# Performance work log

Measured on AMD Instinct MI355X. Metric: run time of the kernel, lower is better.

## Reference

```python
import jax, jax.numpy as jnp
import numpy as np

SLOT_SIZE = 64
START_IDX = 0  # slot2idx['<start>']
STOP_IDX = 1   # slot2idx['<stop>']
NEG_INF = -10000.0


def setup_inputs() -> dict:
    key = jax.random.key(0)
    k1, k2 = jax.random.split(key)
    B, T, S = 512, 512, SLOT_SIZE
    logits = jax.random.normal(k1, (B, T, S), dtype=jnp.float32)
    masks = jnp.ones((B, T), dtype=jnp.float32)
    # nn.Parameter(torch.randn(S, S)) with START/STOP constraints from __init__
    transitions = jax.random.normal(k2, (S, S), dtype=jnp.float32)
    transitions = transitions.at[START_IDX, :].set(NEG_INF)
    transitions = transitions.at[:, STOP_IDX].set(NEG_INF)
    return {"logits": logits, "masks": masks, "transitions": transitions}


def reference(logits, masks, transitions):
    """Faithful CRF.forward == _viterbi_decode(logits, masks).

    Replicates the original quirks:
      - masks multiply only the emission feat (transitions are NOT masked
        inside the Viterbi recursion);
      - path_score is taken from the LAST next_tag's (next_tag = S-1)
        score vector at the final timestep, and the backtrace is seeded
        from that same column's argmax;
      - the backtrace re-applies the last backpointer table once before
        walking backwards (exactly as the torch loop does), and the
        popped start tag is dropped, giving a (B, T-1) path.
    """
    B, T, S = logits.shape
    init = jnp.full((B, S), NEG_INF, dtype=logits.dtype).at[:, START_IDX].set(0.0)

    # masked emissions for timesteps 1..T-1, time-major for scan: (T-1, B, S)
    feats = jnp.swapaxes(logits[:, 1:, :] * masks[:, 1:, None], 0, 1)

    def step(fv, feat_t):
        # scores[b, next, prev] = fv[b, prev] + transitions[next, prev]
        scores = fv[:, None, :] + transitions[None, :, :]  # (B, S, S)
        bptr = jnp.argmax(scores, axis=2).astype(jnp.int32)  # (B, S)
        vmax = jnp.max(scores, axis=2)                       # (B, S)
        return vmax + feat_t, (bptr, vmax)

    _, (bptrs, vmaxs) = jax.lax.scan(step, init, feats)  # (T-1, B, S) each

    # torch quirk: next_tag_var / best_tag_id left over from next_tag = S-1
    path_score = vmaxs[-1][:, S - 1]          # (B,)
    t0 = bptrs[-1][:, S - 1]                  # (B,) seed for backtrace

    def back(tag, bp):
        new_tag = jnp.take_along_axis(bp, tag[:, None], axis=1)[:, 0]
        return new_tag, tag  # emit the tag BEFORE following the pointer

    # reverse scan walks bptrs from last to first; emitted ys land at their
    # original time index, so ys == reversed best_path (start tag dropped
    # because the final carry -- the start tag -- is never emitted).
    _, ys = jax.lax.scan(back, t0, bptrs, reverse=True)  # (T-1, B)
    best_seq = jnp.swapaxes(ys, 0, 1)  # (B, T-1)
    return path_score, best_seq
```

## Files before the change

### kernel.cpp

```cpp
#include <hip/hip_runtime.h>


constexpr int Bz = 512;
constexpr int Tz = 512;
constexpr int Sz = 64;
constexpr float NEGINF = -10000.0f;

__device__ __forceinline__ float rlf(float x, int lane) {
    return __int_as_float(__builtin_amdgcn_readlane(__float_as_int(x), lane));
}

__global__ __launch_bounds__(256)
void crf_viterbi_kernel(const float* __restrict__ logits,
                        const float* __restrict__ masks,
                        const float* __restrict__ trans,
                        float* __restrict__ out)
{
    const int n = threadIdx.x & 63;
    const int w = threadIdx.x >> 6;
    const int b = blockIdx.x;
    const int pbase = w * 16;

    __shared__ unsigned bp[128 * 64];
    __shared__ float pval[2][4][64];
    __shared__ int   pidx[2][4][64];
    __shared__ float ys[Tz - 1];

    float tr[16];
    const float4* tr4 = reinterpret_cast<const float4*>(trans + n * 64 + pbase);
    #pragma unroll
    for (int k = 0; k < 4; ++k) {
        float4 v = tr4[k];
        tr[4 * k + 0] = v.x;
        tr[4 * k + 1] = v.y;
        tr[4 * k + 2] = v.z;
        tr[4 * k + 3] = v.w;
    }

    float fv = (n == 0) ? 0.0f : NEGINF;

    const float* lgbase = logits + (size_t)b * Tz * Sz;
    const float* mkbase = masks + (size_t)b * Tz;

    float lg_next = lgbase[1 * Sz + n];
    unsigned pk = 0;
    float psc = 0.0f;

    #pragma unroll 4
    for (int i = 0; i < Tz - 1; ++i) {
        float lg = lg_next;
        int t2 = (i + 2 < Tz) ? (i + 2) : (Tz - 1);
        lg_next = lgbase[t2 * Sz + n];
        float mk = mkbase[i + 1];

        float v[16];
        #pragma unroll
        for (int j = 0; j < 16; ++j)
            v[j] = rlf(fv, pbase + j) + tr[j];

        float mv[2];
        int   mi[2];
        #pragma unroll
        for (int c = 0; c < 2; ++c) {
            int p0 = 8 * c;
            mv[c] = v[p0];
            mi[c] = pbase + p0;
            #pragma unroll
            for (int j = 1; j < 8; ++j) {
                float x = v[p0 + j];
                bool gt = x > mv[c];
                mi[c] = gt ? (pbase + p0 + j) : mi[c];
                mv[c] = gt ? x : mv[c];
            }
        }
        {
            bool gt = mv[1] > mv[0];
            mi[0] = gt ? mi[1] : mi[0];
            mv[0] = gt ? mv[1] : mv[0];
        }

        const int buf = i & 1;
        pval[buf][w][n] = mv[0];
        pidx[buf][w][n] = mi[0];
        __syncthreads();

        float c0 = pval[buf][0][n], c1 = pval[buf][1][n];
        float c2 = pval[buf][2][n], c3 = pval[buf][3][n];
        int   j0 = pidx[buf][0][n], j1 = pidx[buf][1][n];
        int   j2 = pidx[buf][2][n], j3 = pidx[buf][3][n];

        bool g1 = c1 > c0;  float m01 = g1 ? c1 : c0;  int k01 = g1 ? j1 : j0;
        bool g3 = c3 > c2;  float m23 = g3 ? c3 : c2;  int k23 = g3 ? j3 : j2;
        bool gm = m23 > m01;
        float maxv = gm ? m23 : m01;
        int   maxi = gm ? k23 : k01;

        if (i == Tz - 2) psc = maxv;

        if (w == 0) {
            pk |= ((unsigned)maxi) << (8 * (i & 3));
            if ((i & 3) == 3) {
                bp[(i >> 2) * 64 + n] = pk;
                pk = 0;
            }
        }
        fv = maxv + lg * mk;
    }
    if (w == 0) bp[127 * 64 + n] = pk;
    if (w == 0 && n == 63) out[b] = psc;

    __syncthreads();

    if (w == 0) {
        unsigned wcur = bp[127 * 64 + n];
        int w127_63 = __builtin_amdgcn_readlane((int)wcur, 63);
        int tag = (w127_63 >> 16) & 255;

        for (int g = 127; g >= 0; --g) {
            unsigned wnext = (g > 0) ? bp[(g - 1) * 64 + n] : 0u;
            int smax = (g == 127) ? 2 : 3;
            for (int s = smax; s >= 0; --s) {
                int idx = 4 * g + s;
                if (n == 0) ys[idx] = (float)tag;
                int wd = __builtin_amdgcn_readlane((int)wcur, tag);
                tag = (wd >> (8 * s)) & 255;
            }
            wcur = wnext;
        }
    }

    __syncthreads();

    float* outseq = out + Bz + (size_t)b * (Tz - 1);
    for (int k = threadIdx.x; k < Tz - 1; k += 256) outseq[k] = ys[k];
}

extern "C" void kernel_launch(void* const* d_in, const int* in_sizes, int n_in,
                              void* d_out, int out_size, void* d_ws, size_t ws_size,
                              hipStream_t stream) {
    const float* logits = (const float*)d_in[0];
    const float* masks  = (const float*)d_in[1];
    const float* trans  = (const float*)d_in[2];
    float* out = (float*)d_out;
    (void)in_sizes; (void)n_in; (void)out_size; (void)d_ws; (void)ws_size;

    crf_viterbi_kernel<<<dim3(Bz), dim3(256), 0, stream>>>(logits, masks, trans, out);
}
```

Measured before the change: 414.3 us.

## Split Viterbi state ownership across waves and use tree argmax reduction

Each wave now owns a 16-entry slice of the score vector, so the readlane broadcasts index within the wave's own lanes and only that slice is combined after the barrier. The serial 8-long compare chains are replaced by a pairwise tree argmax to shorten the dependency chain per timestep. Value and index are packed into one int2 in shared memory, and logits and masks are prefetched two steps ahead. All waves now write backpointers for their slice. The aim is lower per-step latency on the serial recursion, at the cost of a more intricate lane-to-state mapping.

```diff
diff --git a/kernel.cpp b/kernel.cpp
--- a/kernel.cpp
+++ b/kernel.cpp
@@ -16,98 +16,99 @@
                         const float* __restrict__ trans,
                         float* __restrict__ out)
 {
-    const int n = threadIdx.x & 63;
-    const int w = threadIdx.x >> 6;
-    const int b = blockIdx.x;
-    const int pbase = w * 16;
+    const int n   = threadIdx.x & 63;
+    const int w   = threadIdx.x >> 6;
+    const int b   = blockIdx.x;
+    const int pb  = 16 * w;
+    const int j   = n & 15;
+    const int myn = pb + j;
 
     __shared__ unsigned bp[128 * 64];
-    __shared__ float pval[2][4][64];
-    __shared__ int   pidx[2][4][64];
+    __shared__ int2 pvi[2][4][64];
     __shared__ float ys[Tz - 1];
 
     float tr[16];
-    const float4* tr4 = reinterpret_cast<const float4*>(trans + n * 64 + pbase);
-    #pragma unroll
-    for (int k = 0; k < 4; ++k) {
-        float4 v = tr4[k];
-        tr[4 * k + 0] = v.x;
-        tr[4 * k + 1] = v.y;
-        tr[4 * k + 2] = v.z;
-        tr[4 * k + 3] = v.w;
+    {
+        const float4* tr4 = reinterpret_cast<const float4*>(trans + n * 64 + pb);
+        #pragma unroll
+        for (int k = 0; k < 4; ++k) {
+            float4 t = tr4[k];
+            tr[4 * k + 0] = t.x; tr[4 * k + 1] = t.y;
+            tr[4 * k + 2] = t.z; tr[4 * k + 3] = t.w;
+        }
     }
 
-    float fv = (n == 0) ? 0.0f : NEGINF;
+    float fvj = (myn == 0) ? 0.0f : NEGINF;
 
     const float* lgbase = logits + (size_t)b * Tz * Sz;
     const float* mkbase = masks + (size_t)b * Tz;
 
-    float lg_next = lgbase[1 * Sz + n];
+    float lg0 = lgbase[1 * Sz + myn], lg1 = lgbase[2 * Sz + myn];
+    float mk0 = mkbase[1],            mk1 = mkbase[2];
+
     unsigned pk = 0;
     float psc = 0.0f;
 
     #pragma unroll 4
     for (int i = 0; i < Tz - 1; ++i) {
-        float lg = lg_next;
-        int t2 = (i + 2 < Tz) ? (i + 2) : (Tz - 1);
-        lg_next = lgbase[t2 * Sz + n];
-        float mk = mkbase[i + 1];
-
         float v[16];
         #pragma unroll
-        for (int j = 0; j < 16; ++j)
-            v[j] = rlf(fv, pbase + j) + tr[j];
+        for (int jj = 0; jj < 16; ++jj)
+            v[jj] = rlf(fvj, jj) + tr[jj];
 
-        float mv[2];
-        int   mi[2];
+        float mv[8]; int mi[8];
         #pragma unroll
-        for (int c = 0; c < 2; ++c) {
-            int p0 = 8 * c;
-            mv[c] = v[p0];
-            mi[c] = pbase + p0;
+        for (int c = 0; c < 8; ++c) {
+            bool g = v[2 * c + 1] > v[2 * c];
+            mv[c] = g ? v[2 * c + 1] : v[2 * c];
+            mi[c] = g ? (2 * c + 1) : (2 * c);
+        }
+        #pragma unroll
+        for (int st = 1; st < 8; st <<= 1) {
             #pragma unroll
-            for (int j = 1; j < 8; ++j) {
-                float x = v[p0 + j];
-                bool gt = x > mv[c];
-                mi[c] = gt ? (pbase + p0 + j) : mi[c];
-                mv[c] = gt ? x : mv[c];
+            for (int c = 0; c < 8; c += 2 * st) {
+                bool g = mv[c + st] > mv[c];
+                mv[c] = g ? mv[c + st] : mv[c];
+                mi[c] = g ? mi[c + st] : mi[c];
             }
         }
-        {
-            bool gt = mv[1] > mv[0];
-            mi[0] = gt ? mi[1] : mi[0];
-            mv[0] = gt ? mv[1] : mv[0];
+        pvi[i & 1][w][n] = make_int2(__float_as_int(mv[0]), pb + mi[0]);
+
+        __syncthreads();
+
+        float cv[4]; int ci[4];
+        #pragma unroll
+        for (int q = 0; q < 4; ++q) {
+            int2 p = pvi[i & 1][q][myn];
+            cv[q] = __int_as_float(p.x);
+            ci[q] = p.y;
+        }
+        bool g1 = cv[1] > cv[0];
+        float m01 = g1 ? cv[1] : cv[0];  int k01 = g1 ? ci[1] : ci[0];
+        bool g3 = cv[3] > cv[2];
+        float m23 = g3 ? cv[3] : cv[2];  int k23 = g3 ? ci[3] : ci[2];
+        bool gm = m23 > m01;
+        float m  = gm ? m23 : m01;
+        int   gi = gm ? k23 : k01;
+
+        if (i == Tz - 2) psc = m;
+
+        pk |= ((unsigned)gi) << (8 * (i & 3));
+        if ((i & 3) == 3) {
+            if (n < 16) bp[(i >> 2) * 64 + myn] = pk;
+            pk = 0;
         }
 
-        const int buf = i & 1;
-        pval[buf][w][n] = mv[0];
-        pidx[buf][w][n] = mi[0];
-        __syncthreads();
+        fvj = m + lg0 * mk0;
 
-        float c0 = pval[buf][0][n], c1 = pval[buf][1][n];
-        float c2 = pval[buf][2][n], c3 = pval[buf][3][n];
-        int   j0 = pidx[buf][0][n], j1 = pidx[buf][1][n];
-        int   j2 = pidx[buf][2][n], j3 = pidx[buf][3][n];
+        lg0 = lg1; mk0 = mk1;
+        int tn = (i + 3 < Tz) ? (i + 3) : (Tz - 1);
+        lg1 = lgbase[tn * Sz + myn];
+        mk1 = mkbase[tn];
+    }
 
-        bool g1 = c1 > c0;  float m01 = g1 ? c1 : c0;  int k01 = g1 ? j1 : j0;
-        bool g3 = c3 > c2;  float m23 = g3 ? c3 : c2;  int k23 = g3 ? j3 : j2;
-        bool gm = m23 > m01;
-        float maxv = gm ? m23 : m01;
-        int   maxi = gm ? k23 : k01;
-
-        if (i == Tz - 2) psc = maxv;
-
-        if (w == 0) {
-            pk |= ((unsigned)maxi) << (8 * (i & 3));
-            if ((i & 3) == 3) {
-                bp[(i >> 2) * 64 + n] = pk;
-                pk = 0;
-            }
-        }
-        fv = maxv + lg * mk;
-    }
-    if (w == 0) bp[127 * 64 + n] = pk;
-    if (w == 0 && n == 63) out[b] = psc;
+    if (n < 16) bp[127 * 64 + myn] = pk;
+    if (w == 3 && n == 63) out[b] = psc;
 
     __syncthreads();
 
@@ -128,7 +129,6 @@
             wcur = wnext;
         }
     }
-
     __syncthreads();
 
     float* outseq = out + Bz + (size_t)b * (Tz - 1);
```

New measurement: 479.9 us. 1.16x slower.
